# Optimization experiments

Measured on AMD Instinct MI355X. Metric: run time of the kernel, lower is better.

## Reference

```python
import jax, jax.numpy as jnp
import numpy as np

B, T, HOR, N = 32, 12, 12, 883
D = 10      # embed_dim == time_dim
HID = 64    # rnn_units
OUT = 1     # output_dim
K = 2       # cheb_k: supports [I, A]


def _pdg2(x, e1, e2, E, Wp, bp):
    # x:[B,N,Ci]  e1,e2:[B,N,D]  E:[N,D]  Wp:[D,K,Ci,Co]  bp:[D,Co]
    nv1 = jnp.tanh(E[None] * e1)                      # [B,N,D]
    nv2 = jnp.tanh(E[None] * e2)
    A = jax.nn.softmax(jax.nn.relu(jnp.einsum('bnd,bmd->bnm', nv1, nv2)), axis=-1)
    xg = jnp.stack([x, jnp.einsum('bnm,bmc->bnc', A, x)], axis=2)   # [B,N,K,Ci]
    W = jnp.einsum('bnd,dkio->bnkio', nv1, Wp)        # node/time-adaptive weights
    b = jnp.einsum('bnd,do->bno', nv1, bp)
    return jnp.einsum('bnki,bnkio->bno', xg, W) + b


def _cell(x, h, e1, e2, E, gW, gb, uW, ub):
    xs = jnp.concatenate([x, h], axis=-1)
    zr = jax.nn.sigmoid(_pdg2(xs, e1, e2, E, gW, gb))
    z, r = jnp.split(zr, 2, axis=-1)
    cand = jnp.concatenate([x, z * h], axis=-1)
    hc = jnp.tanh(_pdg2(cand, e1, e2, E, uW, ub))
    return r * h + (1.0 - r) * hc


def setup_inputs() -> dict:
    key = jax.random.key(0)
    ks = jax.random.split(key, 20)
    s = 0.1
    inp = {
        'src_vals': jax.random.normal(ks[0], (B, T, N, 1), jnp.float32),
        'node_emb': s * jax.random.normal(ks[1], (N, D), jnp.float32),
        'tid_emb1': s * jax.random.normal(ks[2], (288, D), jnp.float32),
        'tid_emb2': s * jax.random.normal(ks[3], (288, D), jnp.float32),
        'diw_emb1': s * jax.random.normal(ks[4], (7, D), jnp.float32),
        'diw_emb2': s * jax.random.normal(ks[5], (7, D), jnp.float32),
        'enc_gate_W': s * jax.random.normal(ks[6], (D, K, 1 + HID, 2 * HID), jnp.float32),
        'enc_gate_b': s * jax.random.normal(ks[7], (D, 2 * HID), jnp.float32),
        'enc_upd_W': s * jax.random.normal(ks[8], (D, K, 1 + HID, HID), jnp.float32),
        'enc_upd_b': s * jax.random.normal(ks[9], (D, HID), jnp.float32),
        'dec_gate_W': s * jax.random.normal(ks[10], (D, K, OUT + HID, 2 * HID), jnp.float32),
        'dec_gate_b': s * jax.random.normal(ks[11], (D, 2 * HID), jnp.float32),
        'dec_upd_W': s * jax.random.normal(ks[12], (D, K, OUT + HID, HID), jnp.float32),
        'dec_upd_b': s * jax.random.normal(ks[13], (D, HID), jnp.float32),
        'proj_W': s * jax.random.normal(ks[14], (OUT, HID), jnp.float32),
        'proj_b': jnp.zeros((OUT,), jnp.float32),
        'src_tid': jax.random.randint(ks[15], (B, T, N), 0, 288, jnp.int32),
        'src_diw': jax.random.randint(ks[16], (B, T, N), 0, 7, jnp.int32),
        'tgt_tid': jax.random.randint(ks[17], (B, HOR, N), 0, 288, jnp.int32),
        'tgt_diw': jax.random.randint(ks[18], (B, HOR, N), 0, 7, jnp.int32),
    }
    return inp


def reference(src_vals, node_emb, tid_emb1, tid_emb2, diw_emb1, diw_emb2,
              enc_gate_W, enc_gate_b, enc_upd_W, enc_upd_b,
              dec_gate_W, dec_gate_b, dec_upd_W, dec_upd_b,
              proj_W, proj_b, src_tid, src_diw, tgt_tid, tgt_diw):
    tm = lambda a: jnp.swapaxes(a, 0, 1)   # batch-major -> time-major
    # periodic embeddings (use_week=True -> elementwise product)
    e1_en = tid_emb1[src_tid] * diw_emb1[src_diw]   # [B,T,N,D]
    e2_en = tid_emb2[src_tid] * diw_emb2[src_diw]
    e1_de = tid_emb1[tgt_tid] * diw_emb1[tgt_diw]   # [B,HOR,N,D]
    e2_de = tid_emb2[tgt_tid] * diw_emb2[tgt_diw]

    h0 = jnp.zeros((src_vals.shape[0], node_emb.shape[0], HID), src_vals.dtype)

    def enc_step(h, inp):
        x, e1, e2 = inp
        h = _cell(x, h, e1, e2, node_emb, enc_gate_W, enc_gate_b, enc_upd_W, enc_upd_b)
        return h, None

    h, _ = jax.lax.scan(enc_step, h0, (tm(src_vals), tm(e1_en), tm(e2_en)))

    go0 = jnp.zeros((src_vals.shape[0], node_emb.shape[0], OUT), src_vals.dtype)

    def dec_step(carry, inp):
        h, go = carry
        e1, e2 = inp
        h = _cell(go, h, e1, e2, node_emb, dec_gate_W, dec_gate_b, dec_upd_W, dec_upd_b)
        go = h @ proj_W.T + proj_b
        return (h, go), go

    _, outs = jax.lax.scan(dec_step, (h, go0), (tm(e1_de), tm(e2_de)))
    return jnp.swapaxes(outs, 0, 1)   # [B,HOR,N,OUT]
```

## Files before the change

kernel.cpp:

```cpp
#include <hip/hip_runtime.h>

#define BB 32
#define TSRC 12
#define HORZ 12
#define NN 883
#define DD 10
#define HH 64
#define BN (BB*NN)
#define BNP 28288
#define KF 5
#define NT 14
#define NST (TSRC+HORZ)

typedef __attribute__((ext_vector_type(8))) short short8;
typedef __attribute__((ext_vector_type(4))) float f32x4;

static __device__ __forceinline__ float sigmf(float x) { return 1.f/(1.f + __expf(-x)); }
static __device__ __forceinline__ float tanh_fast(float x) {
  float e = __expf(2.f*x);
  return (e - 1.f) / (e + 1.f);
}
static __device__ __forceinline__ unsigned int bf_hi(float f) {
  unsigned int u = __float_as_uint(f);
  return (u + 0x7fffu + ((u >> 16) & 1u)) >> 16;
}
static __device__ __forceinline__ float bf_f(unsigned int h) {
  return __uint_as_float(h << 16);
}
static __device__ __forceinline__ void lds_load16(const void* g, void* l) {
  __builtin_amdgcn_global_load_lds(
      (const __attribute__((address_space(1))) void*)g,
      (__attribute__((address_space(3))) void*)l, 16, 0, 0);
}

static __device__ __forceinline__ void swz_block(int& b, int& rt) {
  int lin = blockIdx.x + blockIdx.y*NT;
  int c = lin & 7, q = lin >> 3;
  b = c + ((q/NT) << 3);
  rt = q - (q/NT)*NT;
}

static __device__ __forceinline__ void xs_store(unsigned short* chunk, int c, int mm2, float v) {
  int p0 = (c*128 + (mm2 ^ ((c & 7) << 4))) >> 1;
  unsigned int hi = bf_hi(v);
  chunk[p0] = (unsigned short)hi;
  chunk[p0 + 4096] = (unsigned short)bf_hi(v - bf_f(hi));
}

__global__ __launch_bounds__(256) void prep_all(
    const float* __restrict__ tidE1, const float* __restrict__ tidE2,
    const float* __restrict__ diwE1, const float* __restrict__ diwE2,
    const float* __restrict__ nodeE,
    const int* __restrict__ stid, const int* __restrict__ sdiw,
    const int* __restrict__ ttid, const int* __restrict__ tdiw,
    const float* __restrict__ xsrc,
    float* __restrict__ nv1A, float* __restrict__ nv2A,
    unsigned short* __restrict__ XsH, unsigned short* __restrict__ XsZ)
{
  int i = blockIdx.x*256 + threadIdx.x;
  if (i >= BN) return;
  int st = blockIdx.y;
  int b = i / NN, n = i - b*NN;
  const int* tix = (st < TSRC) ? stid : ttid;
  const int* dix = (st < TSRC) ? sdiw : tdiw;
  int t = (st < TSRC) ? st : st - TSRC;
  int gi = (b*TSRC + t)*NN + n;
  int ti = tix[gi]*DD, di = dix[gi]*DD;
  int nE = n*DD;
  float* nv1T = nv1A + (size_t)st*DD*BNP;
  float* nv2T = nv2A + (size_t)st*DD*BNP;
#pragma unroll
  for (int d = 0; d < DD; ++d) {
    float E = nodeE[nE+d];
    nv1T[d*BNP+i] = tanh_fast(E * (tidE1[ti+d] * diwE1[di+d]));
    nv2T[d*BNP+i] = tanh_fast(E * (tidE2[ti+d] * diwE2[di+d]));
  }
  if (st == 0) {
    float xv = xsrc[gi];
    size_t cb = ((size_t)(b*NT + (n >> 6)))*8192;
    int mm = n & 63;
    unsigned int hi = bf_hi(xv);
    unsigned short los = (unsigned short)bf_hi(xv - bf_f(hi));
    XsH[cb + mm] = (unsigned short)hi; XsH[cb + 4096 + mm] = los;
    XsZ[cb + mm] = (unsigned short)hi; XsZ[cb + 4096 + mm] = los;
  }
}

__global__ __launch_bounds__(256) void wsplit_kernel(
    const float* __restrict__ W, const float* __restrict__ bias,
    int NO, unsigned short* __restrict__ Wf)
{
  int i = blockIdx.x*256 + threadIdx.x;
  int total = DD*2*KF*4*NO*8;
  if (i >= total) return;
  int j = i & 7; int r = i >> 3;
  int o = r % NO; r /= NO;
  int quad = r & 3; r >>= 2;
  int kf = r % KF; r /= KF;
  int hl = r & 1; int d = r >> 1;
  int kk = kf*32 + quad*8 + j;
  float v = 0.f;
  if (kk <= 64)       v = W[(size_t)(d*130 + kk)*NO + o];
  else if (kk == 65)  v = bias[d*NO + o];
  else if (kk <= 130) v = W[(size_t)(d*130 + kk - 1)*NO + o];
  unsigned int hi = bf_hi(v);
  Wf[i] = (hl == 0) ? (unsigned short)hi : (unsigned short)bf_hi(v - bf_f(hi));
}


__global__ __launch_bounds__(256,3) void attn_gate(
    const float* __restrict__ nv1T, const float* __restrict__ nv2T,
    const unsigned short* __restrict__ Xs,
    const float* __restrict__ h,
    const unsigned short* __restrict__ Wf,
    float* __restrict__ rbuf,
    unsigned short* __restrict__ XsZ, float* __restrict__ zh63)
{
  __shared__ float nv1s[DD][64];
  __shared__ float linv[64];
  __shared__ alignas(16) unsigned char U[46080];
  unsigned short* XT = (unsigned short*)U;
  unsigned short* PT = (unsigned short*)(U + 16384);
  float* nv2s = (float*)(U + 34816);
  float* xcolb = (float*)(U + 39936);
  int b, rt;
  swz_block(b, rt);
  int r0 = rt*64;
  int tid = threadIdx.x;
  int rg = tid >> 4, cg = tid & 15;
  int base = b*NN;
  int lane = tid & 63, lm = lane & 15, quad = lane >> 4;
  int w = tid >> 6, mp = w >> 1, np = w & 1;
  const unsigned short* XsB = Xs + (size_t)b*NT*8192;

  for (int idx = tid; idx < DD*64; idx += 256) {
    int d = idx >> 6, r = idx & 63;
    nv1s[d][r] = (r0 + r < NN) ? nv1T[d*BNP + base + r0 + r] : 0.f;
  }

  int4 xt[4];
  float nvr[3]; float xcr;
  {
    const int4* s0 = (const int4*)XsB;
#pragma unroll
    for (int i = 0; i < 4; ++i) xt[i] = s0[w*64 + lane + i*256];
#pragma unroll
    for (int i = 0; i < 3; ++i) {
      int idx = tid + i*256; float v = 0.f;
      if (idx < DD*64) { int d = idx>>6, m = idx&63; v = (m < NN) ? nv2T[d*BNP + base + m] : 0.f; }
      nvr[i] = v;
    }
    xcr = (tid < 64 && tid < NN) ? h[(size_t)63*BNP + base + tid] : 0.f;
#pragma unroll
    for (int i = 0; i < 4; ++i)
      *(int4*)((char*)XT + w*1024 + lane*16 + i*4096) = xt[i];
#pragma unroll
    for (int i = 0; i < 3; ++i) {
      int idx = tid + i*256;
      if (idx < DD*64) nv2s[idx] = nvr[i];
    }
    if (tid < 64) xcolb[tid] = xcr;
  }
  __syncthreads();

  f32x4 accv[2][2] = {};
  float acclp[4] = {}, acc5p[4] = {};

  for (int tI = 0; tI < NT; ++tI) {
    int cur = tI & 1, nxt = cur ^ 1;
    int m0 = tI*64, m0n = m0 + 64;
    bool hasn = tI < NT-1;
    if (hasn) {
      const int4* src = (const int4*)(XsB + (size_t)(tI+1)*8192);
// ... 53 lines not shown
    {
      short8 Aa[2][2], Ab[2][2], Ba[2][2], Bb[2][2];
#pragma unroll
      for (int mt = 0; mt < 2; ++mt) {
        int r = mp*32 + mt*16 + lm;
#pragma unroll
        for (int kf = 0; kf < 2; ++kf) {
          Aa[mt][kf] = *(const short8*)&PT[r*72 + quad*8 + kf*32];
          Ab[mt][kf] = *(const short8*)&PT[64*72 + r*72 + quad*8 + kf*32];
        }
      }
#pragma unroll
      for (int ntl = 0; ntl < 2; ++ntl) {
        int c = np*32 + ntl*16 + lm;
        int swz = (c & 7) << 4;
        int cb0 = c*128 + quad*16;
#pragma unroll
        for (int kf = 0; kf < 2; ++kf) {
          int a = (cb0 + kf*64) ^ swz;
          Ba[ntl][kf] = *(const short8*)((const char*)XT + a);
          Bb[ntl][kf] = *(const short8*)((const char*)XT + a + 8192);
        }
      }
#pragma unroll
      for (int kf = 0; kf < 2; ++kf)
#pragma unroll
        for (int mt = 0; mt < 2; ++mt)
#pragma unroll
          for (int ntl = 0; ntl < 2; ++ntl) {
            accv[mt][ntl] = __builtin_amdgcn_mfma_f32_16x16x32_bf16(Aa[mt][kf], Ba[ntl][kf], accv[mt][ntl], 0,0,0);
            accv[mt][ntl] = __builtin_amdgcn_mfma_f32_16x16x32_bf16(Aa[mt][kf], Bb[ntl][kf], accv[mt][ntl], 0,0,0);
            accv[mt][ntl] = __builtin_amdgcn_mfma_f32_16x16x32_bf16(Ab[mt][kf], Ba[ntl][kf], accv[mt][ntl], 0,0,0);
          }
    }
    if (hasn) {
#pragma unroll
      for (int i = 0; i < 3; ++i) {
        int idx = tid + i*256;
        if (idx < DD*64) nv2s[nxt*(DD*64) + idx] = nvr[i];
      }
      if (tid < 64) xcolb[nxt*64 + tid] = xcr;
    }
    __syncthreads();
    if (hasn) {
#pragma unroll
      for (int i = 0; i < 4; ++i)
        *(int4*)((char*)XT + w*1024 + lane*16 + i*4096) = xt[i];
    }
  }
  int mrow_x = tid >> 2, ksub = tid & 3;
  int gmx = base + r0 + mrow_x;
  const unsigned short* chk_in = Xs + (size_t)(b*NT + rt)*8192;
  int mm2x = mrow_x*2;
  unsigned int pjh[9], pjl[9];
  {
    float r63v = h[(size_t)63*BNP + gmx];
    unsigned int h63 = bf_hi(r63v);
    unsigned int l63 = bf_hi(r63v - bf_f(h63));
#pragma unroll
    for (int i = 0; i < 9; ++i) {
      int kk = ksub*2 + 8*i;
      unsigned int h0 = 0, l0 = 0, h1 = 0, l1 = 0;
      if (kk <= 63) {
        int idx = (kk*128 + (mm2x ^ ((kk & 7) << 4))) >> 1;
        h0 = chk_in[idx]; l0 = chk_in[idx + 4096];
      } else if (kk == 64) { h0 = h63; l0 = l63; }
      int k1 = kk + 1;
      if (kk <= 62) {
        int idx1 = (k1*128 + (mm2x ^ ((k1 & 7) << 4))) >> 1;
        h1 = chk_in[idx1]; l1 = chk_in[idx1 + 4096];
      } else if (k1 == 65) { h1 = 0x3F80u; l1 = 0u; }
      pjh[i] = h0 | (h1 << 16);
      pjl[i] = l0 | (l1 << 16);
    }
  }
#pragma unroll
  for (int off = 1; off <= 8; off <<= 1)
#pragma unroll
    for (int j = 0; j < 4; ++j) {
      acclp[j] += __shfl_xor(acclp[j], off, 64);
      acc5p[j] += __shfl_xor(acc5p[j], off, 64);
    }
  __syncthreads();
  {
    unsigned int* Z = (unsigned int*)(U + 36864);
    for (int idx = tid; idx < 2304; idx += 256) Z[idx] = 0;
  }
  __syncthreads();
  unsigned short* XA = (unsigned short*)U;
  if (cg == 0) {
#pragma unroll
    for (int j = 0; j < 4; ++j) {
      float li = 1.f / acclp[j];
      int r = rg*4 + j;
      linv[r] = li;
      float v = acc5p[j]*li;
      unsigned int hi = bf_hi(v);
      XA[(4*64 + r)*72 + 2] = (unsigned short)hi;
      XA[(4*64 + r)*72 + 32 + 2] = (unsigned short)bf_hi(v - bf_f(hi));
    }
  }
  __syncthreads();
#pragma unroll
  for (int mt = 0; mt < 2; ++mt) {
    int rbase = mp*32 + mt*16 + quad*4;
    float4 lv = *(const float4*)&linv[rbase];
    const float* lvp = (const float*)&lv;
#pragma unroll
    for (int ntl = 0; ntl < 2; ++ntl) {
      int c = np*32 + ntl*16 + lm;
      int kk = 66 + c;
      int kf = kk >> 5, kkl = kk & 31;
#pragma unroll
      for (int r4 = 0; r4 < 4; ++r4) {
        float v = accv[mt][ntl][r4] * lvp[r4];
        unsigned int hi = bf_hi(v);
        int p = (kf*64 + rbase + r4)*72 + kkl;
        XA[p] = (unsigned short)hi;
        XA[p + 32] = (unsigned short)bf_hi(v - bf_f(hi));
      }
    }
  }
  {
    unsigned int* X1 = (unsigned int*)U;
#pragma unroll
    for (int i = 0; i < 9; ++i) {
      int kk = ksub*2 + 8*i;
      if (kk > 64) continue;
      int kf = kk >> 5, kkl = kk & 31;
      int dw = (kf*64 + mrow_x)*36 + (kkl >> 1);
      X1[dw] = pjh[i];
      X1[dw + 16] = pjl[i];
    }
  }
  __syncthreads();
  short8 A1[2][KF], A2[2][KF];
#pragma unroll
  for (int mt = 0; mt < 2; ++mt) {
    int mrow = mp*32 + mt*16 + lm;
#pragma unroll
    for (int kf = 0; kf < KF; ++kf) {
      A1[mt][kf] = *(const short8*)&XA[(kf*64 + mrow)*72 + quad*8];
      A2[mt][kf] = *(const short8*)&XA[(kf*64 + mrow)*72 + 32 + quad*8];
    }
  }
  __syncthreads();
  unsigned char* bufA = U;
  unsigned char* bufB = U + 20480;
  const int colb = np*32 + lm;
#pragma unroll 1
  for (int co = 0; co < 2; ++co) {
    int co0 = co*64;
    {
      const unsigned short* src = Wf + ((size_t)(w*5)*128 + co0)*8 + lane*8;
#pragma unroll
      for (int i = 0; i < 5; ++i)
        lds_load16(src + (size_t)i*128*8, bufA + (w*5+i)*1024);
    }
    f32x4 accO[2][2] = {};
#pragma unroll 1
    for (int d = 0; d < DD; ++d) {
      f32x4 td[2][2] = {};
      __syncthreads();
      {
        const unsigned short* src = Wf + ((size_t)((d*2+1)*20 + w*5)*128 + co0)*8 + lane*8;
#pragma unroll
        for (int i = 0; i < 5; ++i)
          lds_load16(src + (size_t)i*128*8, bufB + (w*5+i)*1024);
      }
#pragma unroll
      for (int kf = 0; kf < KF; ++kf) {
        int cb = ((kf*4 + quad)*64 + colb)*16;
#pragma unroll
        for (int ntl = 0; ntl < 2; ++ntl) {
          short8 Bh = *(const short8*)(bufA + cb + ntl*256);
          td[0][ntl] = __builtin_amdgcn_mfma_f32_16x16x32_bf16(A1[0][kf], Bh, td[0][ntl], 0,0,0);
          td[0][ntl] = __builtin_amdgcn_mfma_f32_16x16x32_bf16(A2[0][kf], Bh, td[0][ntl], 0,0,0);
          td[1][ntl] = __builtin_amdgcn_mfma_f32_16x16x32_bf16(A1[1][kf], Bh, td[1][ntl], 0,0,0);
          td[1][ntl] = __builtin_amdgcn_mfma_f32_16x16x32_bf16(A2[1][kf], Bh, td[1][ntl], 0,0,0);
        }
      }
      __syncthreads();
      if (d < DD-1) {
        const unsigned short* src = Wf + ((size_t)((d+1)*2*20 + w*5)*128 + co0)*8 + lane*8;
#pragma unroll
        for (int i = 0; i < 5; ++i)
          lds_load16(src + (size_t)i*128*8, bufA + (w*5+i)*1024);
      }
#pragma unroll
      for (int kf = 0; kf < KF; ++kf) {
        int cb = ((kf*4 + quad)*64 + colb)*16;
#pragma unroll
        for (int ntl = 0; ntl < 2; ++ntl) {
          short8 Bl = *(const short8*)(bufB + cb + ntl*256);
          td[0][ntl] = __builtin_amdgcn_mfma_f32_16x16x32_bf16(A1[0][kf], Bl, td[0][ntl], 0,0,0);
          td[1][ntl] = __builtin_amdgcn_mfma_f32_16x16x32_bf16(A1[1][kf], Bl, td[1][ntl], 0,0,0);
        }
      }
#pragma unroll
      for (int mt = 0; mt < 2; ++mt) {
        float4 nv4 = *(const float4*)&nv1s[d][mp*32 + mt*16 + quad*4];
        const float* nvp = (const float*)&nv4;
#pragma unroll
        for (int ntl = 0; ntl < 2; ++ntl)
#pragma unroll
          for (int r = 0; r < 4; ++r)
            accO[mt][ntl][r] += nvp[r] * td[mt][ntl][r];
      }
    }
    float* CT = (float*)U;
    __syncthreads();
#pragma unroll
    for (int mt = 0; mt < 2; ++mt)
#pragma unroll
      for (int ntl = 0; ntl < 2; ++ntl)
#pragma unroll
        for (int r = 0; r < 4; ++r)
          CT[(mp*32 + mt*16 + quad*4 + r)*67 + np*32 + ntl*16 + lm] = accO[mt][ntl][r];
    __syncthreads();
    {
      int mm = tid & 63, og = tid >> 6;
      int n = r0 + mm;
      int gm = base + n;
      bool okn = n < NN;
      if (co == 0) {
        unsigned short* chk = XsZ + ((size_t)(b*NT + rt))*8192;
        int mm2 = mm*2;
        for (int j = 0; j < 16; ++j) {
          int o = og*16 + j;
          float z = sigmf(CT[mm*67 + o]);
          float zhv = z * h[(size_t)o*BNP + gm];
          if (okn) {
            if (o < 63) xs_store(chk, o + 1, mm2, zhv);
            else zh63[gm] = zhv;
          }
        }
      } else {
        for (int j = 0; j < 16; ++j) {
          int o = og*16 + j;
          if (okn) rbuf[(size_t)o*BNP + gm] = sigmf(CT[mm*67 + o]);
        }
      }
    }
    __syncthreads();
  }
}

__global__ __launch_bounds__(256,3) void attn_upd(
    const float* __restrict__ nv1T, const float* __restrict__ nv2T,
    const unsigned short* __restrict__ Xs,
    const float* __restrict__ zh63,
    float* __restrict__ hstate,
    const unsigned short* __restrict__ Wf,
    const float* __restrict__ rbuf,
    int dec, const float* __restrict__ pW, const float* __restrict__ pb,
    float* __restrict__ go, float* __restrict__ dout,
    unsigned short* __restrict__ XsH, int t,
    const float* __restrict__ xsrc, int xnmode, int xnt,
    unsigned short* __restrict__ XsZm)
{
  __shared__ float nv1s[DD][64];
  __shared__ float linv[64];
  __shared__ alignas(16) unsigned char U[46080];
  unsigned short* XT = (unsigned short*)U;
  unsigned short* PT = (unsigned short*)(U + 16384);
  float* nv2s = (float*)(U + 34816);
  float* xcolb = (float*)(U + 39936);
  int b, rt;
  swz_block(b, rt);
  int r0 = rt*64;
  int tid = threadIdx.x;
  int rg = tid >> 4, cg = tid & 15;
  int base = b*NN;
  int lane = tid & 63, lm = lane & 15, quad = lane >> 4;
  int w = tid >> 6, mp = w >> 1, np = w & 1;
  const unsigned short* XsB = Xs + (size_t)b*NT*8192;

  for (int idx = tid; idx < DD*64; idx += 256) {
    int d = idx >> 6, r = idx & 63;
    nv1s[d][r] = (r0 + r < NN) ? nv1T[d*BNP + base + r0 + r] : 0.f;
  }

  int4 xt[4];
  float nvr[3]; float xcr;
  {
    const int4* s0 = (const int4*)XsB;
#pragma unroll
    for (int i = 0; i < 4; ++i) xt[i] = s0[w*64 + lane + i*256];
#pragma unroll
    for (int i = 0; i < 3; ++i) {
      int idx = tid + i*256; float v = 0.f;
      if (idx < DD*64) { int d = idx>>6, m = idx&63; v = (m < NN) ? nv2T[d*BNP + base + m] : 0.f; }
      nvr[i] = v;
    }
    xcr = (tid < 64 && tid < NN) ? zh63[base + tid] : 0.f;
#pragma unroll
    for (int i = 0; i < 4; ++i)
      *(int4*)((char*)XT + w*1024 + lane*16 + i*4096) = xt[i];
#pragma unroll
    for (int i = 0; i < 3; ++i) {
      int idx = tid + i*256;
      if (idx < DD*64) nv2s[idx] = nvr[i];
    }
    if (tid < 64) xcolb[tid] = xcr;
  }
  __syncthreads();

  f32x4 accv[2][2] = {};
  float acclp[4] = {}, acc5p[4] = {};

  for (int tI = 0; tI < NT; ++tI) {
    int cur = tI & 1, nxt = cur ^ 1;
    int m0 = tI*64, m0n = m0 + 64;
    bool hasn = tI < NT-1;
    if (hasn) {
      const int4* src = (const int4*)(XsB + (size_t)(tI+1)*8192);
// ... 53 lines not shown
    {
      short8 Aa[2][2], Ab[2][2], Ba[2][2], Bb[2][2];
#pragma unroll
      for (int mt = 0; mt < 2; ++mt) {
        int r = mp*32 + mt*16 + lm;
#pragma unroll
        for (int kf = 0; kf < 2; ++kf) {
          Aa[mt][kf] = *(const short8*)&PT[r*72 + quad*8 + kf*32];
          Ab[mt][kf] = *(const short8*)&PT[64*72 + r*72 + quad*8 + kf*32];
        }
      }
#pragma unroll
      for (int ntl = 0; ntl < 2; ++ntl) {
        int c = np*32 + ntl*16 + lm;
        int swz = (c & 7) << 4;
        int cb0 = c*128 + quad*16;
#pragma unroll
        for (int kf = 0; kf < 2; ++kf) {
          int a = (cb0 + kf*64) ^ swz;
          Ba[ntl][kf] = *(const short8*)((const char*)XT + a);
          Bb[ntl][kf] = *(const short8*)((const char*)XT + a + 8192);
        }
      }
#pragma unroll
      for (int kf = 0; kf < 2; ++kf)
#pragma unroll
        for (int mt = 0; mt < 2; ++mt)
#pragma unroll
          for (int ntl = 0; ntl < 2; ++ntl) {
            accv[mt][ntl] = __builtin_amdgcn_mfma_f32_16x16x32_bf16(Aa[mt][kf], Ba[ntl][kf], accv[mt][ntl], 0,0,0);
            accv[mt][ntl] = __builtin_amdgcn_mfma_f32_16x16x32_bf16(Aa[mt][kf], Bb[ntl][kf], accv[mt][ntl], 0,0,0);
            accv[mt][ntl] = __builtin_amdgcn_mfma_f32_16x16x32_bf16(Ab[mt][kf], Ba[ntl][kf], accv[mt][ntl], 0,0,0);
          }
    }
    if (hasn) {
#pragma unroll
      for (int i = 0; i < 3; ++i) {
        int idx = tid + i*256;
        if (idx < DD*64) nv2s[nxt*(DD*64) + idx] = nvr[i];
      }
      if (tid < 64) xcolb[nxt*64 + tid] = xcr;
    }
    __syncthreads();
    if (hasn) {
#pragma unroll
      for (int i = 0; i < 4; ++i)
        *(int4*)((char*)XT + w*1024 + lane*16 + i*4096) = xt[i];
    }
  }
  int mrow_x = tid >> 2, ksub = tid & 3;
  int gmx = base + r0 + mrow_x;
  const unsigned short* chk_in = Xs + (size_t)(b*NT + rt)*8192;
  int mm2x = mrow_x*2;
  unsigned int pjh[9], pjl[9];
  {
    float r63v = zh63[gmx];
    unsigned int h63 = bf_hi(r63v);
    unsigned int l63 = bf_hi(r63v - bf_f(h63));
#pragma unroll
    for (int i = 0; i < 9; ++i) {
      int kk = ksub*2 + 8*i;
      unsigned int h0 = 0, l0 = 0, h1 = 0, l1 = 0;
      if (kk <= 63) {
        int idx = (kk*128 + (mm2x ^ ((kk & 7) << 4))) >> 1;
        h0 = chk_in[idx]; l0 = chk_in[idx + 4096];
      } else if (kk == 64) { h0 = h63; l0 = l63; }
      int k1 = kk + 1;
      if (kk <= 62) {
        int idx1 = (k1*128 + (mm2x ^ ((k1 & 7) << 4))) >> 1;
        h1 = chk_in[idx1]; l1 = chk_in[idx1 + 4096];
      } else if (k1 == 65) { h1 = 0x3F80u; l1 = 0u; }
      pjh[i] = h0 | (h1 << 16);
      pjl[i] = l0 | (l1 << 16);
    }
  }
#pragma unroll
  for (int off = 1; off <= 8; off <<= 1)
#pragma unroll
    for (int j = 0; j < 4; ++j) {
      acclp[j] += __shfl_xor(acclp[j], off, 64);
      acc5p[j] += __shfl_xor(acc5p[j], off, 64);
    }
  __syncthreads();
  {
    unsigned int* Z = (unsigned int*)(U + 36864);
    for (int idx = tid; idx < 2304; idx += 256) Z[idx] = 0;
  }
  __syncthreads();
  unsigned short* XA = (unsigned short*)U;
  if (cg == 0) {
#pragma unroll
    for (int j = 0; j < 4; ++j) {
      float li = 1.f / acclp[j];
      int r = rg*4 + j;
      linv[r] = li;
      float v = acc5p[j]*li;
      unsigned int hi = bf_hi(v);
      XA[(4*64 + r)*72 + 2] = (unsigned short)hi;
      XA[(4*64 + r)*72 + 32 + 2] = (unsigned short)bf_hi(v - bf_f(hi));
    }
  }
  __syncthreads();
#pragma unroll
  for (int mt = 0; mt < 2; ++mt) {
    int rbase = mp*32 + mt*16 + quad*4;
    float4 lv = *(const float4*)&linv[rbase];
    const float* lvp = (const float*)&lv;
#pragma unroll
    for (int ntl = 0; ntl < 2; ++ntl) {
      int c = np*32 + ntl*16 + lm;
      int kk = 66 + c;
      int kf = kk >> 5, kkl = kk & 31;
#pragma unroll
      for (int r4 = 0; r4 < 4; ++r4) {
        float v = accv[mt][ntl][r4] * lvp[r4];
        unsigned int hi = bf_hi(v);
        int p = (kf*64 + rbase + r4)*72 + kkl;
        XA[p] = (unsigned short)hi;
        XA[p + 32] = (unsigned short)bf_hi(v - bf_f(hi));
      }
    }
  }
  {
    unsigned int* X1 = (unsigned int*)U;
#pragma unroll
    for (int i = 0; i < 9; ++i) {
      int kk = ksub*2 + 8*i;
      if (kk > 64) continue;
      int kf = kk >> 5, kkl = kk & 31;
      int dw = (kf*64 + mrow_x)*36 + (kkl >> 1);
      X1[dw] = pjh[i];
      X1[dw + 16] = pjl[i];
    }
  }
  __syncthreads();
  short8 A1[2][KF], A2[2][KF];
#pragma unroll
  for (int mt = 0; mt < 2; ++mt) {
    int mrow = mp*32 + mt*16 + lm;
#pragma unroll
    for (int kf = 0; kf < KF; ++kf) {
      A1[mt][kf] = *(const short8*)&XA[(kf*64 + mrow)*72 + quad*8];
      A2[mt][kf] = *(const short8*)&XA[(kf*64 + mrow)*72 + 32 + quad*8];
    }
  }
  __syncthreads();
  unsigned char* bufA = U;
  unsigned char* bufB = U + 20480;
  const int colb = np*32 + lm;
  {
    const unsigned short* src = Wf + (size_t)(w*5)*64*8 + lane*8;
#pragma unroll
    for (int i = 0; i < 5; ++i)
      lds_load16(src + (size_t)i*64*8, bufA + (w*5+i)*1024);
  }
  f32x4 accO[2][2] = {};
#pragma unroll 1
  for (int d = 0; d < DD; ++d) {
    f32x4 td[2][2] = {};
    __syncthreads();
    {
      const unsigned short* src = Wf + (size_t)((d*2+1)*20 + w*5)*64*8 + lane*8;
#pragma unroll
      for (int i = 0; i < 5; ++i)
        lds_load16(src + (size_t)i*64*8, bufB + (w*5+i)*1024);
    }
#pragma unroll
    for (int kf = 0; kf < KF; ++kf) {
      int cb = ((kf*4 + quad)*64 + colb)*16;
#pragma unroll
      for (int ntl = 0; ntl < 2; ++ntl) {
        short8 Bh = *(const short8*)(bufA + cb + ntl*256);
        td[0][ntl] = __builtin_amdgcn_mfma_f32_16x16x32_bf16(A1[0][kf], Bh, td[0][ntl], 0,0,0);
        td[0][ntl] = __builtin_amdgcn_mfma_f32_16x16x32_bf16(A2[0][kf], Bh, td[0][ntl], 0,0,0);
        td[1][ntl] = __builtin_amdgcn_mfma_f32_16x16x32_bf16(A1[1][kf], Bh, td[1][ntl], 0,0,0);
        td[1][ntl] = __builtin_amdgcn_mfma_f32_16x16x32_bf16(A2[1][kf], Bh, td[1][ntl], 0,0,0);
      }
    }
    __syncthreads();
    if (d < DD-1) {
      const unsigned short* src = Wf + (size_t)((d+1)*2*20 + w*5)*64*8 + lane*8;
#pragma unroll
      for (int i = 0; i < 5; ++i)
        lds_load16(src + (size_t)i*64*8, bufA + (w*5+i)*1024);
    }
#pragma unroll
    for (int kf = 0; kf < KF; ++kf) {
      int cb = ((kf*4 + quad)*64 + colb)*16;
#pragma unroll
      for (int ntl = 0; ntl < 2; ++ntl) {
        short8 Bl = *(const short8*)(bufB + cb + ntl*256);
        td[0][ntl] = __builtin_amdgcn_mfma_f32_16x16x32_bf16(A1[0][kf], Bl, td[0][ntl], 0,0,0);
        td[1][ntl] = __builtin_amdgcn_mfma_f32_16x16x32_bf16(A1[1][kf], Bl, td[1][ntl], 0,0,0);
      }
    }
#pragma unroll
    for (int mt = 0; mt < 2; ++mt) {
      float4 nv4 = *(const float4*)&nv1s[d][mp*32 + mt*16 + quad*4];
      const float* nvp = (const float*)&nv4;
#pragma unroll
      for (int ntl = 0; ntl < 2; ++ntl)
#pragma unroll
        for (int r = 0; r < 4; ++r)
          accO[mt][ntl][r] += nvp[r] * td[mt][ntl][r];
    }
  }
  float* CT = (float*)U;
  __syncthreads();
#pragma unroll
  for (int mt = 0; mt < 2; ++mt)
#pragma unroll
    for (int ntl = 0; ntl < 2; ++ntl)
#pragma unroll
      for (int r = 0; r < 4; ++r)
        CT[(mp*32 + mt*16 + quad*4 + r)*67 + np*32 + ntl*16 + lm] = accO[mt][ntl][r];
  __syncthreads();
  {
    int mm = tid & 63, og = tid >> 6;
    int n = r0 + mm;
    int gm = base + n;
    bool okn = n < NN;
    unsigned short* chk = XsH + ((size_t)(b*NT + rt))*8192;
    int mm2 = mm*2;
    float pp = 0.f;
    float sval = 0.f;
    for (int j = 0; j < 16; ++j) {
      int o = og*16 + j;
      float hc = tanhf(CT[mm*67 + o]);
      float r = rbuf[(size_t)o*BNP + gm];
      float hv = hstate[(size_t)o*BNP + gm];
      float hn = r*hv + (1.f - r)*hc;
      if (okn) {
        hstate[(size_t)o*BNP + gm] = hn;
        if (o < 63) xs_store(chk, o + 1, mm2, hn);
      }
      if (dec) pp = fmaf(hn, pW[o], pp);
    }
    if (dec) {
      float* PS = CT + 64*67;
      __syncthreads();
      PS[mm*4 + og] = pp;
      __syncthreads();
      if (tid < 64) {
        int n2 = r0 + tid;
        if (n2 < NN) {
          float s = pb[0] + PS[tid*4] + PS[tid*4+1] + PS[tid*4+2] + PS[tid*4+3];
          go[base + n2] = s;
          dout[(b*HORZ + t)*NN + n2] = s;
          sval = s;
        }
      }
    }
    if (xnmode) {
      if (tid < 64) {
        int n2 = r0 + tid;
        if (n2 < NN) {
          float xn;
          if (xnmode == 1)      xn = xsrc[(b*TSRC + xnt)*NN + n2];
          else if (xnmode == 2) xn = 0.f;
          else                  xn = sval;
          unsigned int hix = bf_hi(xn);
          unsigned short lox = (unsigned short)bf_hi(xn - bf_f(hix));
          unsigned short* cH = XsH + ((size_t)(b*NT + rt))*8192;
          unsigned short* cZ = XsZm + ((size_t)(b*NT + rt))*8192;
          cH[tid] = (unsigned short)hix; cH[4096 + tid] = lox;
          cZ[tid] = (unsigned short)hix; cZ[4096 + tid] = lox;
        }
      }
    }
  }
}

extern "C" void kernel_launch(void* const* d_in, const int* in_sizes, int n_in,
                              void* d_out, int out_size, void* d_ws, size_t ws_size,
                              hipStream_t stream) {
  (void)in_sizes; (void)n_in; (void)out_size; (void)ws_size;
  const float* src_vals = (const float*)d_in[0];
  const float* node_emb = (const float*)d_in[1];
  const float* tid1 = (const float*)d_in[2];
  const float* tid2 = (const float*)d_in[3];
  const float* diw1 = (const float*)d_in[4];
  const float* diw2 = (const float*)d_in[5];
  const float* egW = (const float*)d_in[6];
  const float* egb = (const float*)d_in[7];
  const float* euW = (const float*)d_in[8];
  const float* eub = (const float*)d_in[9];
  const float* dgW = (const float*)d_in[10];
  const float* dgb = (const float*)d_in[11];
  const float* duW = (const float*)d_in[12];
  const float* dub = (const float*)d_in[13];
  const float* pW  = (const float*)d_in[14];
  const float* pb  = (const float*)d_in[15];
  const int* stid = (const int*)d_in[16];
  const int* sdiw = (const int*)d_in[17];
  const int* ttid = (const int*)d_in[18];
  const int* tdiw = (const int*)d_in[19];
  float* out = (float*)d_out;

  float* wp = (float*)d_ws;
  float* hbuf = wp; wp += (size_t)64*BNP;
  float* zh63 = wp; wp += BNP + 64;
  float* rbuf = wp; wp += (size_t)64*BNP;
  float* nv1A = wp; wp += (size_t)NST*DD*BNP;
  float* nv2A = wp; wp += (size_t)NST*DD*BNP;
  float* go   = wp; wp += BN + 64;
  unsigned short* egS = (unsigned short*)wp; wp += 204800;
  unsigned short* dgS = (unsigned short*)wp; wp += 204800;
  unsigned short* euS = (unsigned short*)wp; wp += 102400;
  unsigned short* duS = (unsigned short*)wp; wp += 102400;
  unsigned short* XsH = (unsigned short*)wp; wp += 1835008;
  unsigned short* XsZ = (unsigned short*)wp; wp += 1835008;

  hipMemsetAsync(hbuf, 0, sizeof(float)*(size_t)64*BNP, stream);
  hipMemsetAsync(go, 0, sizeof(float)*(BN+64), stream);
  hipMemsetAsync(XsH, 0, (size_t)BB*NT*16384, stream);
  hipMemsetAsync(XsZ, 0, (size_t)BB*NT*16384, stream);

  wsplit_kernel<<<1600,256,0,stream>>>(egW, egb, 128, egS);
  wsplit_kernel<<<1600,256,0,stream>>>(dgW, dgb, 128, dgS);
  wsplit_kernel<<<800,256,0,stream>>>(euW, eub, 64, euS);
  wsplit_kernel<<<800,256,0,stream>>>(duW, dub, 64, duS);

  dim3 pgrid(111, NST);
  prep_all<<<pgrid,256,0,stream>>>(tid1,tid2,diw1,diw2,node_emb,stid,sdiw,ttid,tdiw,src_vals,nv1A,nv2A,XsH,XsZ);

  dim3 fgrid(NT, BB);
  for (int t = 0; t < TSRC; ++t) {
    const float* n1 = nv1A + (size_t)t*DD*BNP;
    const float* n2 = nv2A + (size_t)t*DD*BNP;
    attn_gate<<<fgrid,256,0,stream>>>(n1,n2,XsH,hbuf,egS,rbuf,XsZ,zh63);
    int xnm = (t < TSRC-1) ? 1 : 2;
    attn_upd<<<fgrid,256,0,stream>>>(n1,n2,XsZ,zh63,hbuf,euS,rbuf,0,pW,pb,go,out,XsH,t,src_vals,xnm,t+1,XsZ);
  }
  for (int t = 0; t < HORZ; ++t) {
    const float* n1 = nv1A + (size_t)(TSRC+t)*DD*BNP;
    const float* n2 = nv2A + (size_t)(TSRC+t)*DD*BNP;
    attn_gate<<<fgrid,256,0,stream>>>(n1,n2,XsH,hbuf,dgS,rbuf,XsZ,zh63);
    int xnm = (t < HORZ-1) ? 3 : 0;
    attn_upd<<<fgrid,256,0,stream>>>(n1,n2,XsZ,zh63,hbuf,duS,rbuf,1,pW,pb,go,out,XsH,t,src_vals,xnm,0,XsZ);
  }
}
```

Measured before the change: 4.376 ms.

## Split x/Ax/bias channels to scalar FMA, shrink MFMA K to 128, drop LDS weight staging

```diff
diff --git a/kernel.cpp b/kernel.cpp
--- a/kernel.cpp
+++ b/kernel.cpp
@@ -8,7 +8,7 @@
 #define HH 64
 #define BN (BB*NN)
 #define BNP 28288
-#define KF 5
+#define KF 4
 #define NT 14
 #define NST (TSRC+HORZ)
 
@@ -26,11 +26,6 @@
 }
 static __device__ __forceinline__ float bf_f(unsigned int h) {
   return __uint_as_float(h << 16);
-}
-static __device__ __forceinline__ void lds_load16(const void* g, void* l) {
-  __builtin_amdgcn_global_load_lds(
-      (const __attribute__((address_space(1))) void*)g,
-      (__attribute__((address_space(3))) void*)l, 16, 0, 0);
 }
 
 static __device__ __forceinline__ void swz_block(int& b, int& rt) {
@@ -90,21 +85,35 @@
     const float* __restrict__ W, const float* __restrict__ bias,
     int NO, unsigned short* __restrict__ Wf)
 {
+  (void)bias;
   int i = blockIdx.x*256 + threadIdx.x;
   int total = DD*2*KF*4*NO*8;
   if (i >= total) return;
   int j = i & 7; int r = i >> 3;
   int o = r % NO; r /= NO;
   int quad = r & 3; r >>= 2;
-  int kf = r % KF; r /= KF;
+  int kf = r & 3; r >>= 2;
   int hl = r & 1; int d = r >> 1;
   int kk = kf*32 + quad*8 + j;
-  float v = 0.f;
-  if (kk <= 64)       v = W[(size_t)(d*130 + kk)*NO + o];
-  else if (kk == 65)  v = bias[d*NO + o];
-  else if (kk <= 130) v = W[(size_t)(d*130 + kk - 1)*NO + o];
+  float v = W[(size_t)(d*130 + kk + 1)*NO + o];
   unsigned int hi = bf_hi(v);
   Wf[i] = (hl == 0) ? (unsigned short)hi : (unsigned short)bf_hi(v - bf_f(hi));
+}
+
+__global__ __launch_bounds__(256) void waux_kernel(
+    const float* __restrict__ W, const float* __restrict__ bias,
+    int NO, float* __restrict__ WfA)
+{
+  int i = blockIdx.x*256 + threadIdx.x;
+  int total = DD*3*NO;
+  if (i >= total) return;
+  int o = i % NO; int r = i / NO;
+  int ch = r % 3; int d = r / 3;
+  float v;
+  if (ch == 0)      v = W[(size_t)(d*130 + 0)*NO + o];
+  else if (ch == 1) v = W[(size_t)(d*130 + 129)*NO + o];
+  else              v = bias[d*NO + o];
+  WfA[i] = v;
 }
 
 
@@ -113,12 +122,15 @@
     const unsigned short* __restrict__ Xs,
     const float* __restrict__ h,
     const unsigned short* __restrict__ Wf,
+    const float* __restrict__ WfA,
     float* __restrict__ rbuf,
     unsigned short* __restrict__ XsZ, float* __restrict__ zh63)
 {
   __shared__ float nv1s[DD][64];
   __shared__ float linv[64];
-  __shared__ alignas(16) unsigned char U[46080];
+  __shared__ float xrow[64];
+  __shared__ float ax64r[64];
+  __shared__ alignas(16) unsigned char U[40448];
   unsigned short* XT = (unsigned short*)U;
   unsigned short* PT = (unsigned short*)(U + 16384);
   float* nv2s = (float*)(U + 34816);
@@ -278,24 +290,21 @@
   int gmx = base + r0 + mrow_x;
   const unsigned short* chk_in = Xs + (size_t)(b*NT + rt)*8192;
   int mm2x = mrow_x*2;
-  unsigned int pjh[9], pjl[9];
+  unsigned int pjh[8], pjl[8];
   {
     float r63v = h[(size_t)63*BNP + gmx];
     unsigned int h63 = bf_hi(r63v);
     unsigned int l63 = bf_hi(r63v - bf_f(h63));
 #pragma unroll
-    for (int i = 0; i < 9; ++i) {
+    for (int i = 0; i < 8; ++i) {
       int kk = ksub*2 + 8*i;
-      unsigned int h0 = 0, l0 = 0, h1 = 0, l1 = 0;
-      if (kk <= 63) {
-        int idx = (kk*128 + (mm2x ^ ((kk & 7) << 4))) >> 1;
-        h0 = chk_in[idx]; l0 = chk_in[idx + 4096];
-      } else if (kk == 64) { h0 = h63; l0 = l63; }
+      int c0 = kk + 1;
+      int idx0 = (c0*128 + (mm2x ^ ((c0 & 7) << 4))) >> 1;
+      unsigned int h0 = chk_in[idx0], l0 = chk_in[idx0 + 4096];
+      unsigned int h1, l1;
       int k1 = kk + 1;
-      if (kk <= 62) {
-        int idx1 = (k1*128 + (mm2x ^ ((k1 & 7) << 4))) >> 1;
-        h1 = chk_in[idx1]; l1 = chk_in[idx1 + 4096];
-      } else if (k1 == 65) { h1 = 0x3F80u; l1 = 0u; }
+      if (k1 == 63) { h1 = h63; l1 = l63; }
+      else { int c1 = k1 + 1; int idx1 = (c1*128 + (mm2x ^ ((c1 & 7) << 4))) >> 1; h1 = chk_in[idx1]; l1 = chk_in[idx1 + 4096]; }
       pjh[i] = h0 | (h1 << 16);
       pjl[i] = l0 | (l1 << 16);
     }
@@ -307,11 +316,6 @@
       acclp[j] += __shfl_xor(acclp[j], off, 64);
       acc5p[j] += __shfl_xor(acc5p[j], off, 64);
     }
-  __syncthreads();
-  {
-    unsigned int* Z = (unsigned int*)(U + 36864);
-    for (int idx = tid; idx < 2304; idx += 256) Z[idx] = 0;
-  }
   __syncthreads();
   unsigned short* XA = (unsigned short*)U;
   if (cg == 0) {
@@ -320,12 +324,10 @@
       float li = 1.f / acclp[j];
       int r = rg*4 + j;
       linv[r] = li;
-      float v = acc5p[j]*li;
-      unsigned int hi = bf_hi(v);
-      XA[(4*64 + r)*72 + 2] = (unsigned short)hi;
-      XA[(4*64 + r)*72 + 32 + 2] = (unsigned short)bf_hi(v - bf_f(hi));
-    }
-  }
+      ax64r[r] = acc5p[j]*li;
+    }
+  }
+  if (tid < 64) xrow[tid] = bf_f(chk_in[tid]) + bf_f(chk_in[4096 + tid]);
   __syncthreads();
 #pragma unroll
   for (int mt = 0; mt < 2; ++mt) {
@@ -335,7 +337,7 @@
 #pragma unroll
     for (int ntl = 0; ntl < 2; ++ntl) {
       int c = np*32 + ntl*16 + lm;
-      int kk = 66 + c;
+      int kk = 64 + c;
       int kf = kk >> 5, kkl = kk & 31;
 #pragma unroll
       for (int r4 = 0; r4 < 4; ++r4) {
@@ -350,9 +352,8 @@
   {
     unsigned int* X1 = (unsigned int*)U;
 #pragma unroll
-    for (int i = 0; i < 9; ++i) {
+    for (int i = 0; i < 8; ++i) {
       int kk = ksub*2 + 8*i;
-      if (kk > 64) continue;
       int kf = kk >> 5, kkl = kk & 31;
       int dw = (kf*64 + mrow_x)*36 + (kkl >> 1);
       X1[dw] = pjh[i];
@@ -370,68 +371,58 @@
       A2[mt][kf] = *(const short8*)&XA[(kf*64 + mrow)*72 + 32 + quad*8];
     }
   }
-  __syncthreads();
-  unsigned char* bufA = U;
-  unsigned char* bufB = U + 20480;
+  float xvr[2][4], avr[2][4];
+#pragma unroll
+  for (int mt = 0; mt < 2; ++mt) {
+    float4 xq = *(const float4*)&xrow[mp*32 + mt*16 + quad*4];
+    float4 aq = *(const float4*)&ax64r[mp*32 + mt*16 + quad*4];
+    xvr[mt][0]=xq.x; xvr[mt][1]=xq.y; xvr[mt][2]=xq.z; xvr[mt][3]=xq.w;
+    avr[mt][0]=aq.x; avr[mt][1]=aq.y; avr[mt][2]=aq.z; avr[mt][3]=aq.w;
+  }
   const int colb = np*32 + lm;
 #pragma unroll 1
   for (int co = 0; co < 2; ++co) {
     int co0 = co*64;
-    {
-      const unsigned short* src = Wf + ((size_t)(w*5)*128 + co0)*8 + lane*8;
-#pragma unroll
-      for (int i = 0; i < 5; ++i)
-        lds_load16(src + (size_t)i*128*8, bufA + (w*5+i)*1024);
-    }
+    int cA0 = co0 + colb, cA1 = cA0 + 16;
     f32x4 accO[2][2] = {};
 #pragma unroll 1
     for (int d = 0; d < DD; ++d) {
       f32x4 td[2][2] = {};
-      __syncthreads();
-      {
-        const unsigned short* src = Wf + ((size_t)((d*2+1)*20 + w*5)*128 + co0)*8 + lane*8;
-#pragma unroll
-        for (int i = 0; i < 5; ++i)
-          lds_load16(src + (size_t)i*128*8, bufB + (w*5+i)*1024);
-      }
+      float wx0 = WfA[(d*3+0)*128 + cA0], wx1 = WfA[(d*3+0)*128 + cA1];
+      float wa0 = WfA[(d*3+1)*128 + cA0], wa1 = WfA[(d*3+1)*128 + cA1];
+      float wb0 = WfA[(d*3+2)*128 + cA0], wb1 = WfA[(d*3+2)*128 + cA1];
 #pragma unroll
       for (int kf = 0; kf < KF; ++kf) {
-        int cb = ((kf*4 + quad)*64 + colb)*16;
-#pragma unroll
-        for (int ntl = 0; ntl < 2; ++ntl) {
-          short8 Bh = *(const short8*)(bufA + cb + ntl*256);
-          td[0][ntl] = __builtin_amdgcn_mfma_f32_16x16x32_bf16(A1[0][kf], Bh, td[0][ntl], 0,0,0);
-          td[0][ntl] = __builtin_amdgcn_mfma_f32_16x16x32_bf16(A2[0][kf], Bh, td[0][ntl], 0,0,0);
-          td[1][ntl] = __builtin_amdgcn_mfma_f32_16x16x32_bf16(A1[1][kf], Bh, td[1][ntl], 0,0,0);
-          td[1][ntl] = __builtin_amdgcn_mfma_f32_16x16x32_bf16(A2[1][kf], Bh, td[1][ntl], 0,0,0);
-        }
-      }
-      __syncthreads();
-      if (d < DD-1) {
-        const unsigned short* src = Wf + ((size_t)((d+1)*2*20 + w*5)*128 + co0)*8 + lane*8;
-#pragma unroll
-        for (int i = 0; i < 5; ++i)
-          lds_load16(src + (size_t)i*128*8, bufA + (w*5+i)*1024);
-      }
-#pragma unroll
-      for (int kf = 0; kf < KF; ++kf) {
-        int cb = ((kf*4 + quad)*64 + colb)*16;
-#pragma unroll
-        for (int ntl = 0; ntl < 2; ++ntl) {
-          short8 Bl = *(const short8*)(bufB + cb + ntl*256);
-          td[0][ntl] = __builtin_amdgcn_mfma_f32_16x16x32_bf16(A1[0][kf], Bl, td[0][ntl], 0,0,0);
-          td[1][ntl] = __builtin_amdgcn_mfma_f32_16x16x32_bf16(A1[1][kf], Bl, td[1][ntl], 0,0,0);
-        }
+        size_t obh = (((size_t)(d*2+0)*4 + kf)*4 + quad)*128;
+        size_t obl = (((size_t)(d*2+1)*4 + kf)*4 + quad)*128;
+        short8 Bh0 = *(const short8*)(Wf + (obh + cA0)*8);
+        short8 Bh1 = *(const short8*)(Wf + (obh + cA1)*8);
+        short8 Bl0 = *(const short8*)(Wf + (obl + cA0)*8);
+        short8 Bl1 = *(const short8*)(Wf + (obl + cA1)*8);
+        td[0][0] = __builtin_amdgcn_mfma_f32_16x16x32_bf16(A1[0][kf], Bh0, td[0][0], 0,0,0);
+        td[0][0] = __builtin_amdgcn_mfma_f32_16x16x32_bf16(A2[0][kf], Bh0, td[0][0], 0,0,0);
+        td[1][0] = __builtin_amdgcn_mfma_f32_16x16x32_bf16(A1[1][kf], Bh0, td[1][0], 0,0,0);
+        td[1][0] = __builtin_amdgcn_mfma_f32_16x16x32_bf16(A2[1][kf], Bh0, td[1][0], 0,0,0);
+        td[0][0] = __builtin_amdgcn_mfma_f32_16x16x32_bf16(A1[0][kf], Bl0, td[0][0], 0,0,0);
+        td[1][0] = __builtin_amdgcn_mfma_f32_16x16x32_bf16(A1[1][kf], Bl0, td[1][0], 0,0,0);
+        td[0][1] = __builtin_amdgcn_mfma_f32_16x16x32_bf16(A1[0][kf], Bh1, td[0][1], 0,0,0);
+        td[0][1] = __builtin_amdgcn_mfma_f32_16x16x32_bf16(A2[0][kf], Bh1, td[0][1], 0,0,0);
+        td[1][1] = __builtin_amdgcn_mfma_f32_16x16x32_bf16(A1[1][kf], Bh1, td[1][1], 0,0,0);
+        td[1][1] = __builtin_amdgcn_mfma_f32_16x16x32_bf16(A2[1][kf], Bh1, td[1][1], 0,0,0);
+        td[0][1] = __builtin_amdgcn_mfma_f32_16x16x32_bf16(A1[0][kf], Bl1, td[0][1], 0,0,0);
+        td[1][1] = __builtin_amdgcn_mfma_f32_16x16x32_bf16(A1[1][kf], Bl1, td[1][1], 0,0,0);
       }
 #pragma unroll
       for (int mt = 0; mt < 2; ++mt) {
         float4 nv4 = *(const float4*)&nv1s[d][mp*32 + mt*16 + quad*4];
         const float* nvp = (const float*)&nv4;
 #pragma unroll
-        for (int ntl = 0; ntl < 2; ++ntl)
-#pragma unroll
-          for (int r = 0; r < 4; ++r)
-            accO[mt][ntl][r] += nvp[r] * td[mt][ntl][r];
+        for (int r = 0; r < 4; ++r) {
+          float t0 = td[mt][0][r] + wb0 + xvr[mt][r]*wx0 + avr[mt][r]*wa0;
+          float t1 = td[mt][1][r] + wb1 + xvr[mt][r]*wx1 + avr[mt][r]*wa1;
+          accO[mt][0][r] += nvp[r] * t0;
+          accO[mt][1][r] += nvp[r] * t1;
+        }
       }
     }
     float* CT = (float*)U;
@@ -478,6 +469,7 @@
     const float* __restrict__ zh63,
     float* __restrict__ hstate,
     const unsigned short* __restrict__ Wf,
+    const float* __restrict__ WfA,
     const float* __restrict__ rbuf,
     int dec, const float* __restrict__ pW, const float* __restrict__ pb,
     float* __restrict__ go, float* __restrict__ dout,
@@ -487,7 +479,9 @@
 {
   __shared__ float nv1s[DD][64];
   __shared__ float linv[64];
-  __shared__ alignas(16) unsigned char U[46080];
+  __shared__ float xrow[64];
+  __shared__ float ax64r[64];
+  __shared__ alignas(16) unsigned char U[40448];
   unsigned short* XT = (unsigned short*)U;
   unsigned short* PT = (unsigned short*)(U + 16384);
   float* nv2s = (float*)(U + 34816);
@@ -647,24 +641,21 @@
   int gmx = base + r0 + mrow_x;
   const unsigned short* chk_in = Xs + (size_t)(b*NT + rt)*8192;
   int mm2x = mrow_x*2;
-  unsigned int pjh[9], pjl[9];
+  unsigned int pjh[8], pjl[8];
   {
     float r63v = zh63[gmx];
     unsigned int h63 = bf_hi(r63v);
     unsigned int l63 = bf_hi(r63v - bf_f(h63));
 #pragma unroll
-    for (int i = 0; i < 9; ++i) {
+    for (int i = 0; i < 8; ++i) {
       int kk = ksub*2 + 8*i;
-      unsigned int h0 = 0, l0 = 0, h1 = 0, l1 = 0;
-      if (kk <= 63) {
-        int idx = (kk*128 + (mm2x ^ ((kk & 7) << 4))) >> 1;
-        h0 = chk_in[idx]; l0 = chk_in[idx + 4096];
-      } else if (kk == 64) { h0 = h63; l0 = l63; }
+      int c0 = kk + 1;
+      int idx0 = (c0*128 + (mm2x ^ ((c0 & 7) << 4))) >> 1;
+      unsigned int h0 = chk_in[idx0], l0 = chk_in[idx0 + 4096];
+      unsigned int h1, l1;
       int k1 = kk + 1;
-      if (kk <= 62) {
-        int idx1 = (k1*128 + (mm2x ^ ((k1 & 7) << 4))) >> 1;
-        h1 = chk_in[idx1]; l1 = chk_in[idx1 + 4096];
-      } else if (k1 == 65) { h1 = 0x3F80u; l1 = 0u; }
+      if (k1 == 63) { h1 = h63; l1 = l63; }
+      else { int c1 = k1 + 1; int idx1 = (c1*128 + (mm2x ^ ((c1 & 7) << 4))) >> 1; h1 = chk_in[idx1]; l1 = chk_in[idx1 + 4096]; }
       pjh[i] = h0 | (h1 << 16);
       pjl[i] = l0 | (l1 << 16);
     }
@@ -676,11 +667,6 @@
       acclp[j] += __shfl_xor(acclp[j], off, 64);
       acc5p[j] += __shfl_xor(acc5p[j], off, 64);
     }
-  __syncthreads();
-  {
-    unsigned int* Z = (unsigned int*)(U + 36864);
-    for (int idx = tid; idx < 2304; idx += 256) Z[idx] = 0;
-  }
   __syncthreads();
   unsigned short* XA = (unsigned short*)U;
   if (cg == 0) {
@@ -689,12 +675,10 @@
       float li = 1.f / acclp[j];
       int r = rg*4 + j;
       linv[r] = li;
-      float v = acc5p[j]*li;
-      unsigned int hi = bf_hi(v);
-      XA[(4*64 + r)*72 + 2] = (unsigned short)hi;
-      XA[(4*64 + r)*72 + 32 + 2] = (unsigned short)bf_hi(v - bf_f(hi));
-    }
-  }
+      ax64r[r] = acc5p[j]*li;
+    }
+  }
+  if (tid < 64) xrow[tid] = bf_f(chk_in[tid]) + bf_f(chk_in[4096 + tid]);
   __syncthreads();
 #pragma unroll
   for (int mt = 0; mt < 2; ++mt) {
@@ -704,7 +688,7 @@
 #pragma unroll
     for (int ntl = 0; ntl < 2; ++ntl) {
       int c = np*32 + ntl*16 + lm;
-      int kk = 66 + c;
+      int kk = 64 + c;
       int kf = kk >> 5, kkl = kk & 31;
 #pragma unroll
       for (int r4 = 0; r4 < 4; ++r4) {
@@ -719,9 +703,8 @@
   {
     unsigned int* X1 = (unsigned int*)U;
 #pragma unroll
-    for (int i = 0; i < 9; ++i) {
+    for (int i = 0; i < 8; ++i) {
       int kk = ksub*2 + 8*i;
-      if (kk > 64) continue;
       int kf = kk >> 5, kkl = kk & 31;
       int dw = (kf*64 + mrow_x)*36 + (kkl >> 1);
       X1[dw] = pjh[i];
@@ -739,65 +722,55 @@
       A2[mt][kf] = *(const short8*)&XA[(kf*64 + mrow)*72 + 32 + quad*8];
     }
   }
-  __syncthreads();
-  unsigned char* bufA = U;
-  unsigned char* bufB = U + 20480;
+  float xvr[2][4], avr[2][4];
+#pragma unroll
+  for (int mt = 0; mt < 2; ++mt) {
+    float4 xq = *(const float4*)&xrow[mp*32 + mt*16 + quad*4];
+    float4 aq = *(const float4*)&ax64r[mp*32 + mt*16 + quad*4];
+    xvr[mt][0]=xq.x; xvr[mt][1]=xq.y; xvr[mt][2]=xq.z; xvr[mt][3]=xq.w;
+    avr[mt][0]=aq.x; avr[mt][1]=aq.y; avr[mt][2]=aq.z; avr[mt][3]=aq.w;
+  }
   const int colb = np*32 + lm;
-  {
-    const unsigned short* src = Wf + (size_t)(w*5)*64*8 + lane*8;
-#pragma unroll
-    for (int i = 0; i < 5; ++i)
-      lds_load16(src + (size_t)i*64*8, bufA + (w*5+i)*1024);
-  }
+  const int cA0 = colb, cA1 = colb + 16;
   f32x4 accO[2][2] = {};
 #pragma unroll 1
   for (int d = 0; d < DD; ++d) {
     f32x4 td[2][2] = {};
-    __syncthreads();
-    {
-      const unsigned short* src = Wf + (size_t)((d*2+1)*20 + w*5)*64*8 + lane*8;
-#pragma unroll
-      for (int i = 0; i < 5; ++i)
-        lds_load16(src + (size_t)i*64*8, bufB + (w*5+i)*1024);
-    }
+    float wx0 = WfA[(d*3+0)*64 + cA0], wx1 = WfA[(d*3+0)*64 + cA1];
+    float wa0 = WfA[(d*3+1)*64 + cA0], wa1 = WfA[(d*3+1)*64 + cA1];
+    float wb0 = WfA[(d*3+2)*64 + cA0], wb1 = WfA[(d*3+2)*64 + cA1];
 #pragma unroll
     for (int kf = 0; kf < KF; ++kf) {
-      int cb = ((kf*4 + quad)*64 + colb)*16;
-#pragma unroll
-      for (int ntl = 0; ntl < 2; ++ntl) {
-        short8 Bh = *(const short8*)(bufA + cb + ntl*256);
-        td[0][ntl] = __builtin_amdgcn_mfma_f32_16x16x32_bf16(A1[0][kf], Bh, td[0][ntl], 0,0,0);
-        td[0][ntl] = __builtin_amdgcn_mfma_f32_16x16x32_bf16(A2[0][kf], Bh, td[0][ntl], 0,0,0);
-        td[1][ntl] = __builtin_amdgcn_mfma_f32_16x16x32_bf16(A1[1][kf], Bh, td[1][ntl], 0,0,0);
-        td[1][ntl] = __builtin_amdgcn_mfma_f32_16x16x32_bf16(A2[1][kf], Bh, td[1][ntl], 0,0,0);
-      }
-    }
-    __syncthreads();
-    if (d < DD-1) {
-      const unsigned short* src = Wf + (size_t)((d+1)*2*20 + w*5)*64*8 + lane*8;
-#pragma unroll
-      for (int i = 0; i < 5; ++i)
-        lds_load16(src + (size_t)i*64*8, bufA + (w*5+i)*1024);
-    }
-#pragma unroll
-    for (int kf = 0; kf < KF; ++kf) {
-      int cb = ((kf*4 + quad)*64 + colb)*16;
-#pragma unroll
-      for (int ntl = 0; ntl < 2; ++ntl) {
-        short8 Bl = *(const short8*)(bufB + cb + ntl*256);
-        td[0][ntl] = __builtin_amdgcn_mfma_f32_16x16x32_bf16(A1[0][kf], Bl, td[0][ntl], 0,0,0);
-        td[1][ntl] = __builtin_amdgcn_mfma_f32_16x16x32_bf16(A1[1][kf], Bl, td[1][ntl], 0,0,0);
-      }
+      size_t obh = (((size_t)(d*2+0)*4 + kf)*4 + quad)*64;
+      size_t obl = (((size_t)(d*2+1)*4 + kf)*4 + quad)*64;
+      short8 Bh0 = *(const short8*)(Wf + (obh + cA0)*8);
+      short8 Bh1 = *(const short8*)(Wf + (obh + cA1)*8);
+      short8 Bl0 = *(const short8*)(Wf + (obl + cA0)*8);
+      short8 Bl1 = *(const short8*)(Wf + (obl + cA1)*8);
+      td[0][0] = __builtin_amdgcn_mfma_f32_16x16x32_bf16(A1[0][kf], Bh0, td[0][0], 0,0,0);
+      td[0][0] = __builtin_amdgcn_mfma_f32_16x16x32_bf16(A2[0][kf], Bh0, td[0][0], 0,0,0);
+      td[1][0] = __builtin_amdgcn_mfma_f32_16x16x32_bf16(A1[1][kf], Bh0, td[1][0], 0,0,0);
+      td[1][0] = __builtin_amdgcn_mfma_f32_16x16x32_bf16(A2[1][kf], Bh0, td[1][0], 0,0,0);
+      td[0][0] = __builtin_amdgcn_mfma_f32_16x16x32_bf16(A1[0][kf], Bl0, td[0][0], 0,0,0);
+      td[1][0] = __builtin_amdgcn_mfma_f32_16x16x32_bf16(A1[1][kf], Bl0, td[1][0], 0,0,0);
+      td[0][1] = __builtin_amdgcn_mfma_f32_16x16x32_bf16(A1[0][kf], Bh1, td[0][1], 0,0,0);
+      td[0][1] = __builtin_amdgcn_mfma_f32_16x16x32_bf16(A2[0][kf], Bh1, td[0][1], 0,0,0);
+      td[1][1] = __builtin_amdgcn_mfma_f32_16x16x32_bf16(A1[1][kf], Bh1, td[1][1], 0,0,0);
+      td[1][1] = __builtin_amdgcn_mfma_f32_16x16x32_bf16(A2[1][kf], Bh1, td[1][1], 0,0,0);
+      td[0][1] = __builtin_amdgcn_mfma_f32_16x16x32_bf16(A1[0][kf], Bl1, td[0][1], 0,0,0);
+      td[1][1] = __builtin_amdgcn_mfma_f32_16x16x32_bf16(A1[1][kf], Bl1, td[1][1], 0,0,0);
     }
 #pragma unroll
     for (int mt = 0; mt < 2; ++mt) {
       float4 nv4 = *(const float4*)&nv1s[d][mp*32 + mt*16 + quad*4];
       const float* nvp = (const float*)&nv4;
 #pragma unroll
-      for (int ntl = 0; ntl < 2; ++ntl)
-#pragma unroll
-        for (int r = 0; r < 4; ++r)
-          accO[mt][ntl][r] += nvp[r] * td[mt][ntl][r];
+      for (int r = 0; r < 4; ++r) {
+        float t0 = td[mt][0][r] + wb0 + xvr[mt][r]*wx0 + avr[mt][r]*wa0;
+        float t1 = td[mt][1][r] + wb1 + xvr[mt][r]*wx1 + avr[mt][r]*wa1;
+        accO[mt][0][r] += nvp[r] * t0;
+        accO[mt][1][r] += nvp[r] * t1;
+      }
     }
   }
   float* CT = (float*)U;
@@ -899,10 +872,14 @@
   float* nv1A = wp; wp += (size_t)NST*DD*BNP;
   float* nv2A = wp; wp += (size_t)NST*DD*BNP;
   float* go   = wp; wp += BN + 64;
-  unsigned short* egS = (unsigned short*)wp; wp += 204800;
-  unsigned short* dgS = (unsigned short*)wp; wp += 204800;
-  unsigned short* euS = (unsigned short*)wp; wp += 102400;
-  unsigned short* duS = (unsigned short*)wp; wp += 102400;
+  unsigned short* egS = (unsigned short*)wp; wp += 163840;
+  unsigned short* dgS = (unsigned short*)wp; wp += 163840;
+  unsigned short* euS = (unsigned short*)wp; wp += 81920;
+  unsigned short* duS = (unsigned short*)wp; wp += 81920;
+  float* egA = wp; wp += 3840;
+  float* dgA = wp; wp += 3840;
+  float* euA = wp; wp += 1920;
+  float* duA = wp; wp += 1920;
   unsigned short* XsH = (unsigned short*)wp; wp += 1835008;
   unsigned short* XsZ = (unsigned short*)wp; wp += 1835008;
 
@@ -911,10 +888,14 @@
   hipMemsetAsync(XsH, 0, (size_t)BB*NT*16384, stream);
   hipMemsetAsync(XsZ, 0, (size_t)BB*NT*16384, stream);
 
-  wsplit_kernel<<<1600,256,0,stream>>>(egW, egb, 128, egS);
-  wsplit_kernel<<<1600,256,0,stream>>>(dgW, dgb, 128, dgS);
-  wsplit_kernel<<<800,256,0,stream>>>(euW, eub, 64, euS);
-  wsplit_kernel<<<800,256,0,stream>>>(duW, dub, 64, duS);
+  wsplit_kernel<<<1280,256,0,stream>>>(egW, egb, 128, egS);
+  wsplit_kernel<<<1280,256,0,stream>>>(dgW, dgb, 128, dgS);
+  wsplit_kernel<<<640,256,0,stream>>>(euW, eub, 64, euS);
+  wsplit_kernel<<<640,256,0,stream>>>(duW, dub, 64, duS);
+  waux_kernel<<<15,256,0,stream>>>(egW, egb, 128, egA);
+  waux_kernel<<<15,256,0,stream>>>(dgW, dgb, 128, dgA);
+  waux_kernel<<<8,256,0,stream>>>(euW, eub, 64, euA);
+  waux_kernel<<<8,256,0,stream>>>(duW, dub, 64, duA);
 
   dim3 pgrid(111, NST);
   prep_all<<<pgrid,256,0,stream>>>(tid1,tid2,diw1,diw2,node_emb,stid,sdiw,ttid,tdiw,src_vals,nv1A,nv2A,XsH,XsZ);
@@ -923,15 +904,15 @@
   for (int t = 0; t < TSRC; ++t) {
     const float* n1 = nv1A + (size_t)t*DD*BNP;
     const float* n2 = nv2A + (size_t)t*DD*BNP;
-    attn_gate<<<fgrid,256,0,stream>>>(n1,n2,XsH,hbuf,egS,rbuf,XsZ,zh63);
+    attn_gate<<<fgrid,256,0,stream>>>(n1,n2,XsH,hbuf,egS,egA,rbuf,XsZ,zh63);
     int xnm = (t < TSRC-1) ? 1 : 2;
-    attn_upd<<<fgrid,256,0,stream>>>(n1,n2,XsZ,zh63,hbuf,euS,rbuf,0,pW,pb,go,out,XsH,t,src_vals,xnm,t+1,XsZ);
+    attn_upd<<<fgrid,256,0,stream>>>(n1,n2,XsZ,zh63,hbuf,euS,euA,rbuf,0,pW,pb,go,out,XsH,t,src_vals,xnm,t+1,XsZ);
   }
   for (int t = 0; t < HORZ; ++t) {
     const float* n1 = nv1A + (size_t)(TSRC+t)*DD*BNP;
     const float* n2 = nv2A + (size_t)(TSRC+t)*DD*BNP;
-    attn_gate<<<fgrid,256,0,stream>>>(n1,n2,XsH,hbuf,dgS,rbuf,XsZ,zh63);
+    attn_gate<<<fgrid,256,0,stream>>>(n1,n2,XsH,hbuf,dgS,dgA,rbuf,XsZ,zh63);
     int xnm = (t < HORZ-1) ? 3 : 0;
-    attn_upd<<<fgrid,256,0,stream>>>(n1,n2,XsZ,zh63,hbuf,duS,rbuf,1,pW,pb,go,out,XsH,t,src_vals,xnm,0,XsZ);
-  }
-}
+    attn_upd<<<fgrid,256,0,stream>>>(n1,n2,XsZ,zh63,hbuf,duS,duA,rbuf,1,pW,pb,go,out,XsH,t,src_vals,xnm,0,XsZ);
+  }
+}
```

Result: slower. 5.499 ms (+25.6%).
